# Kernel optimization log

Hardware: AMD Instinct MI355X
Metric: run time of the kernel (lower is better)

Reference implementation:

```python
import jax, jax.numpy as jnp
import numpy as np

B, NP, D, K, H = 2, 512, 768, 64, 8
HD = D // H  # head dim = 96


def layernorm(x, g, b, eps=1e-5):
    m = jnp.mean(x, axis=-1, keepdims=True)
    v = jnp.mean((x - m) ** 2, axis=-1, keepdims=True)
    return (x - m) / jnp.sqrt(v + eps) * g + b


def setup_inputs() -> dict:
    key = jax.random.key(0)
    ks = jax.random.split(key, 16)
    s = 0.02
    return {
        "features": jax.random.normal(ks[0], (B, NP, D), jnp.float32),
        "points_xyz": jax.random.normal(ks[1], (B, NP, 3), jnp.float32),
        # distance_encoder: Linear(1 -> D)
        "Wd": jax.random.normal(ks[2], (D,), jnp.float32) * s,
        "bd": jnp.zeros((D,), jnp.float32),
        # geo_attention: MultiheadAttention(D, H)
        "Wq": jax.random.normal(ks[3], (D, D), jnp.float32) * s,
        "bq": jnp.zeros((D,), jnp.float32),
        "Wk": jax.random.normal(ks[4], (D, D), jnp.float32) * s,
        "bk": jnp.zeros((D,), jnp.float32),
        "Wv": jax.random.normal(ks[5], (D, D), jnp.float32) * s,
        "bv": jnp.zeros((D,), jnp.float32),
        "Wo": jax.random.normal(ks[6], (D, D), jnp.float32) * s,
        "bo": jnp.zeros((D,), jnp.float32),
        # spatial_enhancer: Linear(2D -> D) + LayerNorm + SiLU
        "We": jax.random.normal(ks[7], (2 * D, D), jnp.float32) * s,
        "be": jnp.zeros((D,), jnp.float32),
        "g_ln": jnp.ones((D,), jnp.float32),
        "b_ln": jnp.zeros((D,), jnp.float32),
    }


def reference(features, points_xyz, Wd, bd, Wq, bq, Wk, bk, Wv, bv, Wo, bo, We, be, g_ln, b_ln):
    # pairwise distances per batch: [B, Np, Np]
    sq = jnp.sum(points_xyz ** 2, axis=-1)
    d2 = sq[:, :, None] + sq[:, None, :] - 2.0 * jnp.einsum("bnd,bmd->bnm", points_xyz, points_xyz)
    dist = jnp.sqrt(jnp.maximum(d2, 0.0))
    # k nearest neighbors (smallest distances)
    neg_d, idx = jax.lax.top_k(-dist, K)          # idx: [B, Np, K]
    nbr_dist = -neg_d                              # [B, Np, K]
    # gather neighbor features: [B, Np, K, D]
    nbr_feat = jax.vmap(lambda f, i: f[i])(features, idx)
    # distance encoder: Linear(1->D) on unsqueezed distances
    dist_feat = nbr_dist[..., None] * Wd + bd      # [B, Np, K, D]
    kv = nbr_feat + dist_feat
    # multi-head attention: per-point query over its K neighbors
    q = (features @ Wq + bq).reshape(B, NP, H, HD)
    k = (kv @ Wk + bk).reshape(B, NP, K, H, HD)
    v = (kv @ Wv + bv).reshape(B, NP, K, H, HD)
    scores = jnp.einsum("bnhd,bnkhd->bnhk", q, k) / jnp.sqrt(jnp.float32(HD))
    attn = jax.nn.softmax(scores, axis=-1)
    o = jnp.einsum("bnhk,bnkhd->bnhd", attn, v).reshape(B, NP, D)
    attended = o @ Wo + bo                          # [B, Np, D]
    # spatial enhancer on [features ; attended]
    ctx = jnp.concatenate([features, attended], axis=-1)
    enhanced = jax.nn.silu(layernorm(ctx @ We + be, g_ln, b_ln))
    return enhanced
```

## Files before the change

### kernel.cpp

```cpp
#include <hip/hip_runtime.h>
#include <math.h>

#define NPTS 512
#define DIM  768
#define KNN  64
#define NH   8
#define HDIM 96
#define MROWS 1024
#define MPAD  1088
#define WOROWS 832
#define WSQ   ((size_t)DIM * DIM)

typedef unsigned short u16;
typedef __attribute__((ext_vector_type(8))) short short8;
typedef __attribute__((ext_vector_type(4))) float f32x4;

__device__ __forceinline__ unsigned f2bf(float f) {
    unsigned u = __float_as_uint(f);
    return (u + 0x7fffu + ((u >> 16) & 1u)) >> 16;
}
__device__ __forceinline__ float bf2f(u16 v) {
    return __uint_as_float(((unsigned)v) << 16);
}

__global__ __launch_bounds__(256) void mega_prep_k(
    const float* __restrict__ features,
    const float* __restrict__ Wd, const float* __restrict__ bd,
    const float* __restrict__ Wq, const float* __restrict__ Wk, const float* __restrict__ Wv,
    const float* __restrict__ Wo, const float* __restrict__ bo, const float* __restrict__ We,
    u16* __restrict__ Fb, u16* __restrict__ Wob, u16* __restrict__ W3)
{
    __shared__ float T[64][65];
    int bid = blockIdx.x, tid = threadIdx.x;

    if (bid < 768) {
        int i = (bid * 256 + tid) * 4;
        float4 v = *(const float4*)&features[i];
        uint2 o;
        o.x = f2bf(v.x) | (f2bf(v.y) << 16);
        o.y = f2bf(v.z) | (f2bf(v.w) << 16);
        *(uint2*)&Fb[i] = o;
        return;
    }
    if (bid < 816) {
        int flat = (bid - 768) * 1024 + tid * 4;
        int r = flat / DIM, c = flat - r * DIM;
        uint2 o; o.x = 0u; o.y = 0u;
        if (r == 0) {
            float4 v = *(const float4*)&Wd[c];
            o.x = f2bf(v.x) | (f2bf(v.y) << 16);
            o.y = f2bf(v.z) | (f2bf(v.w) << 16);
        } else if (r == 1) {
            float4 v = *(const float4*)&bd[c];
            o.x = f2bf(v.x) | (f2bf(v.y) << 16);
            o.y = f2bf(v.z) | (f2bf(v.w) << 16);
        }
        *(uint2*)&Fb[(size_t)(MROWS + r) * DIM + c] = o;
        return;
    }
    if (bid < 1440) {
        int flat = (bid - 816) * 1024 + tid * 4;
        int r = flat / DIM, c = flat - r * DIM;
        uint2 o; o.x = 0u; o.y = 0u;
        if (r < DIM) {
            float4 v = *(const float4*)&Wo[(size_t)r * DIM + c];
            o.x = f2bf(v.x) | (f2bf(v.y) << 16);
            o.y = f2bf(v.z) | (f2bf(v.w) << 16);
        } else if (r == DIM) {
            float4 v = *(const float4*)&bo[c];
            o.x = f2bf(v.x) | (f2bf(v.y) << 16);
            o.y = f2bf(v.z) | (f2bf(v.w) << 16);
        }
        *(uint2*)&Wob[(size_t)r * DIM + c] = o;
        return;
    }
    {
        int t = bid - 1440;
        int m = t / 144, r2 = t % 144;
        int by = r2 / 12, bx = r2 % 12;
        const float* S = (m == 0) ? Wq : (m == 1) ? Wk : (m == 2) ? Wv
                       : (m == 3) ? We : (We + WSQ);
        u16* D = W3 + (size_t)m * WSQ;
        int r0 = by * 64, c0 = bx * 64;
#pragma unroll
        for (int i = 0; i < 16; ++i) {
            int lin = tid + i * 256;
            int r = lin >> 6, c = lin & 63;
            T[r][c] = S[(size_t)(r0 + r) * DIM + c0 + c];
        }
        __syncthreads();
#pragma unroll
        for (int i = 0; i < 16; ++i) {
            int lin = tid + i * 256;
            int c = lin >> 6, r = lin & 63;
            D[(size_t)(c0 + c) * DIM + r0 + r] = (u16)f2bf(T[r][c]);
        }
    }
}

union alignas(16) GTSm {
    struct { short As[64][72]; short Bs[64][72]; } g;
    struct { float P[NPTS * 3]; unsigned long long keys[NPTS]; } tk;
};

__global__ __launch_bounds__(256) void qkvw_topk_k(
    const u16* __restrict__ Fb, const u16* __restrict__ Wob, const u16* __restrict__ W3,
    const float* __restrict__ bq, const float* __restrict__ pts,
    float* __restrict__ FQ, u16* __restrict__ FKb, u16* __restrict__ FVb,
    u16* __restrict__ WeffT, float* __restrict__ c_e,
    int* __restrict__ idxb, float* __restrict__ distb)
{
    __shared__ GTSm sm;
    int bid = blockIdx.x, tid = threadIdx.x;

    if (bid >= 816) {
        int bn = bid - 816;
        int b  = bn >> 9;
        int n  = bn & (NPTS - 1);
        const float* pb = pts + (size_t)b * NPTS * 3;
        for (int i = tid; i < NPTS * 3; i += 256) sm.tk.P[i] = pb[i];
        __syncthreads();
        float xn = sm.tk.P[n * 3], yn = sm.tk.P[n * 3 + 1], zn = sm.tk.P[n * 3 + 2];
        float sqn = xn * xn + yn * yn + zn * zn;
        for (int m = tid; m < NPTS; m += 256) {
            float xm = sm.tk.P[m * 3], ym = sm.tk.P[m * 3 + 1], zm = sm.tk.P[m * 3 + 2];
            float sqm = xm * xm + ym * ym + zm * zm;
            float d2 = sqn + sqm - 2.0f * (xn * xm + yn * ym + zn * zm);
            float dist = sqrtf(fmaxf(d2, 0.0f));
            sm.tk.keys[m] = (((unsigned long long)__float_as_uint(dist)) << 32) | (unsigned)m;
        }
        __syncthreads();
        for (int k = 2; k <= NPTS; k <<= 1) {
            for (int j = k >> 1; j > 0; j >>= 1) {
                for (int i = tid; i < NPTS; i += 256) {
                    int ixj = i ^ j;
                    if (ixj > i) {
                        bool asc = ((i & k) == 0);
                        unsigned long long a = sm.tk.keys[i], bb = sm.tk.keys[ixj];
                        if ((a > bb) == asc) { sm.tk.keys[i] = bb; sm.tk.keys[ixj] = a; }
                    }
                }
                __syncthreads();
            }
        }
        if (tid < KNN) {
            unsigned long long kk = sm.tk.keys[tid];
            idxb[(size_t)bn * KNN + tid]  = (int)(kk & 0xffffffffu);
            distb[(size_t)bn * KNN + tid] = __uint_as_float((unsigned)(kk >> 32));
        }
        return;
    }

    int z   = bid / 204;
    int rem = bid - z * 204;
    int by  = rem / 12;
    int bx  = rem - by * 12;
    if (z == 0 && by >= 16) return;
    if (z == 3 && by >= 13) return;
    const u16* A  = (z == 3) ? Wob : Fb;
    const u16* BT = W3 + (size_t)((z == 3) ? 4 : z) * WSQ;

    int wave = tid >> 6, lane = tid & 63;
    int wr = (wave >> 1) * 32, wc = (wave & 1) * 32;
    int l15 = lane & 15, kg = lane >> 4;
    int brow = by * 64, bcol = bx * 64;

    f32x4 acc[2][2] = {};

    int srow = tid >> 3;
    int scol = (tid & 7) * 8;

    for (int k0 = 0; k0 < DIM; k0 += 64) {
#pragma unroll
        for (int s = 0; s < 2; ++s) {
            int r = srow + s * 32;
            *(short8*)&sm.g.As[r][scol] = *(const short8*)&A[(size_t)(brow + r) * DIM + k0 + scol];
            *(short8*)&sm.g.Bs[r][scol] = *(const short8*)&BT[(size_t)(bcol + r) * DIM + k0 + scol];
        }
        __syncthreads();
#pragma unroll
        for (int kk = 0; kk < 2; ++kk) {
            short8 a0 = *(const short8*)&sm.g.As[wr + l15][kk * 32 + kg * 8];
            short8 a1 = *(const short8*)&sm.g.As[wr + 16 + l15][kk * 32 + kg * 8];
            short8 b0 = *(const short8*)&sm.g.Bs[wc + l15][kk * 32 + kg * 8];
            short8 b1 = *(const short8*)&sm.g.Bs[wc + 16 + l15][kk * 32 + kg * 8];
            acc[0][0] = __builtin_amdgcn_mfma_f32_16x16x32_bf16(a0, b0, acc[0][0], 0, 0, 0);
            acc[0][1] = __builtin_amdgcn_mfma_f32_16x16x32_bf16(a0, b1, acc[0][1], 0, 0, 0);
            acc[1][0] = __builtin_amdgcn_mfma_f32_16x16x32_bf16(a1, b0, acc[1][0], 0, 0, 0);
            acc[1][1] = __builtin_amdgcn_mfma_f32_16x16x32_bf16(a1, b1, acc[1][1], 0, 0, 0);
        }
        __syncthreads();
    }

#pragma unroll
    for (int m = 0; m < 2; ++m) {
#pragma unroll
        for (int n = 0; n < 2; ++n) {
            int col  = bcol + wc + n * 16 + l15;
            int row0 = brow + wr + m * 16 + kg * 4;
            if (z == 0) {
                float bv = bq[col];
#pragma unroll
                for (int j = 0; j < 4; ++j)
                    FQ[(size_t)(row0 + j) * DIM + col] = acc[m][n][j] + bv;
            } else if (z == 1) {
#pragma unroll
                for (int j = 0; j < 4; ++j)
                    FKb[(size_t)(row0 + j) * DIM + col] = (u16)f2bf(acc[m][n][j]);
            } else if (z == 2) {
#pragma unroll
                for (int j = 0; j < 4; ++j)
                    FVb[(size_t)(row0 + j) * DIM + col] = (u16)f2bf(acc[m][n][j]);
            } else {
                if (row0 + 3 < DIM) {
                    unsigned long long pk =
                          (unsigned long long)f2bf(acc[m][n][0])
                        | ((unsigned long long)f2bf(acc[m][n][1]) << 16)
                        | ((unsigned long long)f2bf(acc[m][n][2]) << 32)
                        | ((unsigned long long)f2bf(acc[m][n][3]) << 48);
                    *(unsigned long long*)&WeffT[(size_t)col * DIM + row0] = pk;
                } else {
#pragma unroll
                    for (int j = 0; j < 4; ++j) {
                        int row = row0 + j;
                        if (row < DIM)       WeffT[(size_t)col * DIM + row] = (u16)f2bf(acc[m][n][j]);
                        else if (row == DIM) c_e[col] = acc[m][n][j];
                    }
                }
            }
        }
    }
}

__global__ __launch_bounds__(256) void gemm_final_k(
    const u16* __restrict__ Fb, const u16* __restrict__ Ob,
    const u16* __restrict__ WeTopT, const u16* __restrict__ WeffT,
    const float* __restrict__ c_e, const float* __restrict__ be,
    float* __restrict__ Z0, float* __restrict__ Z1)
{
    int z = blockIdx.z;
    const u16*   A    = z ? Ob : Fb;
    const u16*   BT   = z ? WeffT : WeTopT;
    const float* bias = z ? c_e : be;
    float*       Z    = z ? Z1 : Z0;

    __shared__ short As[64][72];
    __shared__ short Bs[64][72];

    int tid  = threadIdx.x;
    int wave = tid >> 6, lane = tid & 63;
    int wr = (wave >> 1) * 32, wc = (wave & 1) * 32;
    int l15 = lane & 15, kg = lane >> 4;
    int brow = blockIdx.y * 64, bcol = blockIdx.x * 64;

    f32x4 acc[2][2] = {};

    int srow = tid >> 3;
    int scol = (tid & 7) * 8;

    for (int k0 = 0; k0 < DIM; k0 += 64) {
#pragma unroll
        for (int s = 0; s < 2; ++s) {
            int r = srow + s * 32;
            *(short8*)&As[r][scol] = *(const short8*)&A[(size_t)(brow + r) * DIM + k0 + scol];
            *(short8*)&Bs[r][scol] = *(const short8*)&BT[(size_t)(bcol + r) * DIM + k0 + scol];
        }
        __syncthreads();
#pragma unroll
        for (int kk = 0; kk < 2; ++kk) {
            short8 a0 = *(const short8*)&As[wr + l15][kk * 32 + kg * 8];
            short8 a1 = *(const short8*)&As[wr + 16 + l15][kk * 32 + kg * 8];
            short8 b0 = *(const short8*)&Bs[wc + l15][kk * 32 + kg * 8];
            short8 b1 = *(const short8*)&Bs[wc + 16 + l15][kk * 32 + kg * 8];
            acc[0][0] = __builtin_amdgcn_mfma_f32_16x16x32_bf16(a0, b0, acc[0][0], 0, 0, 0);
            acc[0][1] = __builtin_amdgcn_mfma_f32_16x16x32_bf16(a0, b1, acc[0][1], 0, 0, 0);
            acc[1][0] = __builtin_amdgcn_mfma_f32_16x16x32_bf16(a1, b0, acc[1][0], 0, 0, 0);
            acc[1][1] = __builtin_amdgcn_mfma_f32_16x16x32_bf16(a1, b1, acc[1][1], 0, 0, 0);
        }
        __syncthreads();
    }

#pragma unroll
    for (int m = 0; m < 2; ++m) {
#pragma unroll
        for (int n = 0; n < 2; ++n) {
            int col = bcol + wc + n * 16 + l15;
            float bv = bias[col];
#pragma unroll
            for (int j = 0; j < 4; ++j) {
                int row = brow + wr + m * 16 + kg * 4 + j;
                Z[(size_t)row * DIM + col] = acc[m][n][j] + bv;
            }
        }
    }
}

__global__ __launch_bounds__(512) void attn_k(
    const float* __restrict__ FQ, const u16* __restrict__ FKb, const u16* __restrict__ FVb,
    const int* __restrict__ idxb, const float* __restrict__ distb,
    const float* __restrict__ bk, const float* __restrict__ bv,
    u16* __restrict__ O)
{
    int bn = blockIdx.x;
    int b  = bn >> 9;
    int tid = threadIdx.x;
    int wv = tid >> 6, lane = tid & 63;

    __shared__ float qlds[NH][104];
    __shared__ int   s_idx[KNN];
    __shared__ float s_dist[KNN];
    __shared__ float s_sc[NH][68];
    __shared__ float s_att[NH][68];
    __shared__ float s_qh[NH][2];
    __shared__ float s_sd[NH];

    if (tid < KNN) {
        s_idx[tid]  = idxb[(size_t)bn * KNN + tid];
        s_dist[tid] = distb[(size_t)bn * KNN + tid];
    }
    const float* qrow = FQ + (size_t)bn * DIM;
    {
        int d = tid;
        if (d < DIM) qlds[d / HDIM][d % HDIM] = qrow[d];
        int d2 = tid + 512;
        if (d2 < DIM) qlds[d2 / HDIM][d2 % HDIM] = qrow[d2];
    }
    __syncthreads();

    {
        int h = wv;
        const u16* wdk = FKb + (size_t)MROWS * DIM + h * HDIM;
        const u16* ckr = FKb + (size_t)(MROWS + 1) * DIM + h * HDIM;
        const float* bkh = bk + h * HDIM;
        float q = qlds[h][lane];
        float pw = q * bf2f(wdk[lane]);
        float pc = q * (bf2f(ckr[lane]) + bkh[lane]);
        if (lane < HDIM - 64) {
            float q2 = qlds[h][lane + 64];
            pw = fmaf(q2, bf2f(wdk[lane + 64]), pw);
            pc = fmaf(q2, bf2f(ckr[lane + 64]) + bkh[lane + 64], pc);
        }
#pragma unroll
        for (int off = 32; off; off >>= 1) {
            pw += __shfl_xor(pw, off);
            pc += __shfl_xor(pc, off);
        }
        if (lane == 0) { s_qh[h][0] = pw; s_qh[h][1] = pc; }
    }

    {
        int j = tid >> 3, h = tid & 7;
        const u16* kr = FKb + (size_t)(b * NPTS + s_idx[j]) * DIM + h * HDIM;
        const uint4* kr4 = (const uint4*)kr;
        float a0 = 0.f, a1 = 0.f, a2 = 0.f, a3 = 0.f;
#pragma unroll
        for (int i = 0; i < 12; ++i) {
            uint4 kv = kr4[i];
            float4 qa = *(const float4*)&qlds[h][i * 8];
            float4 qb = *(const float4*)&qlds[h][i * 8 + 4];
            a0 = fmaf(qa.x, __uint_as_float(kv.x << 16), a0);
            a1 = fmaf(qa.y, __uint_as_float(kv.x & 0xffff0000u), a1);
            a2 = fmaf(qa.z, __uint_as_float(kv.y << 16), a2);
            a3 = fmaf(qa.w, __uint_as_float(kv.y & 0xffff0000u), a3);
            a0 = fmaf(qb.x, __uint_as_float(kv.z << 16), a0);
            a1 = fmaf(qb.y, __uint_as_float(kv.z & 0xffff0000u), a1);
            a2 = fmaf(qb.z, __uint_as_float(kv.w << 16), a2);
            a3 = fmaf(qb.w, __uint_as_float(kv.w & 0xffff0000u), a3);
        }
        s_sc[h][j] = (a0 + a1) + (a2 + a3);
    }
    __syncthreads();

    {
        int h = wv, j = lane;
        const float invs = 0.10206207261596575f;
        float qwdk = s_qh[h][0], qck = s_qh[h][1];
        float dj = s_dist[j];
        float sc = (s_sc[h][j] + dj * qwdk + qck) * invs;
        float mx = sc;
#pragma unroll
        for (int off = 32; off; off >>= 1) mx = fmaxf(mx, __shfl_xor(mx, off));
        float ev = __expf(sc - mx);
        float sum = ev;
#pragma unroll
        for (int off = 32; off; off >>= 1) sum += __shfl_xor(sum, off);
        float att = ev / sum;
        s_att[h][j] = att;
        float sd = att * dj;
#pragma unroll
        for (int off = 32; off; off >>= 1) sd += __shfl_xor(sd, off);
        if (lane == 0) s_sd[h] = sd;
    }
    __syncthreads();

    if (tid < 384) {
        int d0 = tid * 2;
        int h  = d0 / HDIM;
        const float* attp = s_att[h];
        const size_t basev = (size_t)(b * NPTS) * DIM + d0;
        float o0 = 0.f, o1 = 0.f;
#pragma unroll 4
        for (int j = 0; j < KNN; ++j) {
            unsigned pv = *(const unsigned*)&FVb[basev + (size_t)s_idx[j] * DIM];
            float a = attp[j];
            o0 = fmaf(a, __uint_as_float(pv << 16), o0);
            o1 = fmaf(a, __uint_as_float(pv & 0xffff0000u), o1);
        }
        const u16* wdv = FVb + (size_t)MROWS * DIM;
        const u16* cvr = FVb + (size_t)(MROWS + 1) * DIM;
        float sdh = s_sd[h];
        o0 += sdh * bf2f(wdv[d0])     + (bf2f(cvr[d0])     + bv[d0]);
        o1 += sdh * bf2f(wdv[d0 + 1]) + (bf2f(cvr[d0 + 1]) + bv[d0 + 1]);
        unsigned po = f2bf(o0) | (f2bf(o1) << 16);
        *(unsigned*)&O[(size_t)bn * DIM + d0] = po;
    }
}

__global__ __launch_bounds__(256) void ln_silu_k(
    const float* __restrict__ Z0, const float* __restrict__ Z1,
    const float* __restrict__ g, const float* __restrict__ bta,
    float* __restrict__ out)
{
    int bn = blockIdx.x, tid = threadIdx.x;
    const float* z0 = Z0 + (size_t)bn * DIM;
    const float* z1 = Z1 + (size_t)bn * DIM;
    int e0 = tid * 3;
    float x0 = z0[e0] + z1[e0];
    float x1 = z0[e0 + 1] + z1[e0 + 1];
    float x2 = z0[e0 + 2] + z1[e0 + 2];
    float s = x0 + x1 + x2;
    float ss = x0 * x0 + x1 * x1 + x2 * x2;
    __shared__ float red[4][2];
#pragma unroll
    for (int off = 32; off; off >>= 1) {
        s  += __shfl_xor(s, off);
        ss += __shfl_xor(ss, off);
    }
    int w = tid >> 6;
    if ((tid & 63) == 0) { red[w][0] = s; red[w][1] = ss; }
    __syncthreads();
    s  = red[0][0] + red[1][0] + red[2][0] + red[3][0];
    ss = red[0][1] + red[1][1] + red[2][1] + red[3][1];
    float mean = s * (1.0f / DIM);
    float var  = ss * (1.0f / DIM) - mean * mean;
    float rstd = rsqrtf(var + 1e-5f);
    float* orow = out + (size_t)bn * DIM;
#pragma unroll
    for (int i = 0; i < 3; ++i) {
        int e = e0 + i;
        float x = (i == 0) ? x0 : (i == 1) ? x1 : x2;
        float y = (x - mean) * rstd * g[e] + bta[e];
        orow[e] = y / (1.0f + __expf(-y));
    }
}

extern "C" void kernel_launch(void* const* d_in, const int* in_sizes, int n_in,
                              void* d_out, int out_size, void* d_ws, size_t ws_size,
                              hipStream_t stream)
{
    const float* features = (const float*)d_in[0];
    const float* pts      = (const float*)d_in[1];
    const float* Wd       = (const float*)d_in[2];
    const float* bd       = (const float*)d_in[3];
    const float* Wq       = (const float*)d_in[4];
    const float* bq       = (const float*)d_in[5];
    const float* Wk       = (const float*)d_in[6];
    const float* bk       = (const float*)d_in[7];
    const float* Wv       = (const float*)d_in[8];
    const float* bv       = (const float*)d_in[9];
    const float* Wo       = (const float*)d_in[10];
    const float* bo       = (const float*)d_in[11];
    const float* We       = (const float*)d_in[12];
    const float* be       = (const float*)d_in[13];
    const float* g_ln     = (const float*)d_in[14];
    const float* b_ln     = (const float*)d_in[15];

    const size_t MAT  = (size_t)MROWS * DIM;
    const size_t MATP = (size_t)MPAD  * DIM;

    float* ws = (float*)d_ws;
    float* FQ    = ws;
    u16*   FKb   = (u16*)(ws + MATP);
    u16*   FVb   = FKb + MATP;
    u16*   Fb    = FVb + MATP;
    u16*   Ob    = Fb + MATP;
    u16*   Wob   = Ob + MAT;
    u16*   W3    = Wob + (size_t)WOROWS * DIM;
    u16*   WeffT = W3 + 5 * WSQ;
    float* c_e   = (float*)(WeffT + WSQ);
    int*   idxb  = (int*)(c_e + DIM);
    float* distb = (float*)(idxb + (size_t)MROWS * KNN);
    float* Z0    = FQ;
    float* Z1    = (float*)FKb;

    mega_prep_k<<<2160, 256, 0, stream>>>(features, Wd, bd, Wq, Wk, Wv, Wo, bo, We,
                                          Fb, Wob, W3);
    qkvw_topk_k<<<1840, 256, 0, stream>>>(
        Fb, Wob, W3, bq, pts, FQ, FKb, FVb, WeffT, c_e, idxb, distb);
    attn_k<<<MROWS, 512, 0, stream>>>(FQ, FKb, FVb, idxb, distb, bk, bv, Ob);
    gemm_final_k<<<dim3(12, 16, 2), 256, 0, stream>>>(
        Fb, Ob, W3 + 3 * WSQ, WeffT, c_e, be, Z0, Z1);
    ln_silu_k<<<MROWS, 256, 0, stream>>>(Z0, Z1, g_ln, b_ln, (float*)d_out);
}
```

Baseline: 78.98 us.

## Move features@We_top GEMM into qkv kernel and split-K the attended GEMM

The Z0 = features·We_top + be GEMM does not depend on attention, so it moves into the earlier qkv/topk kernel as a fifth z-slice, overlapping with the other independent work. The remaining O·Weff GEMM is split four ways along K into separate partial buffers, which gives more blocks on the device. LayerNorm then sums the four partials, Z0 and c_e with float4 loads using 192 threads. This costs extra workspace and extra global traffic for the partial sums.

```diff
diff --git a/kernel.cpp b/kernel.cpp
--- a/kernel.cpp
+++ b/kernel.cpp
@@ -105,16 +105,17 @@
 
 __global__ __launch_bounds__(256) void qkvw_topk_k(
     const u16* __restrict__ Fb, const u16* __restrict__ Wob, const u16* __restrict__ W3,
-    const float* __restrict__ bq, const float* __restrict__ pts,
+    const float* __restrict__ bq, const float* __restrict__ be,
+    const float* __restrict__ pts,
     float* __restrict__ FQ, u16* __restrict__ FKb, u16* __restrict__ FVb,
-    u16* __restrict__ WeffT, float* __restrict__ c_e,
+    u16* __restrict__ WeffT, float* __restrict__ c_e, float* __restrict__ Z0,
     int* __restrict__ idxb, float* __restrict__ distb)
 {
     __shared__ GTSm sm;
     int bid = blockIdx.x, tid = threadIdx.x;
 
-    if (bid >= 816) {
-        int bn = bid - 816;
+    if (bid >= 1008) {
+        int bn = bid - 1008;
         int b  = bn >> 9;
         int n  = bn & (NPTS - 1);
         const float* pb = pts + (size_t)b * NPTS * 3;
@@ -151,14 +152,20 @@
         return;
     }
 
-    int z   = bid / 204;
-    int rem = bid - z * 204;
-    int by  = rem / 12;
-    int bx  = rem - by * 12;
-    if (z == 0 && by >= 16) return;
-    if (z == 3 && by >= 13) return;
+    int z, by, bx;
+    if (bid < 816) {
+        z = bid / 204;
+        int rem = bid - z * 204;
+        by = rem / 12; bx = rem - by * 12;
+        if (z == 0 && by >= 16) return;
+        if (z == 3 && by >= 13) return;
+    } else {
+        z = 4;
+        int rem = bid - 816;
+        by = rem / 12; bx = rem - by * 12;
+    }
     const u16* A  = (z == 3) ? Wob : Fb;
-    const u16* BT = W3 + (size_t)((z == 3) ? 4 : z) * WSQ;
+    const u16* BT = W3 + (size_t)((z == 3) ? 4 : (z == 4) ? 3 : z) * WSQ;
 
     int wave = tid >> 6, lane = tid & 63;
     int wr = (wave >> 1) * 32, wc = (wave & 1) * 32;
@@ -211,6 +218,11 @@
 #pragma unroll
                 for (int j = 0; j < 4; ++j)
                     FVb[(size_t)(row0 + j) * DIM + col] = (u16)f2bf(acc[m][n][j]);
+            } else if (z == 4) {
+                float bv = be[col];
+#pragma unroll
+                for (int j = 0; j < 4; ++j)
+                    Z0[(size_t)(row0 + j) * DIM + col] = acc[m][n][j] + bv;
             } else {
                 if (row0 + 3 < DIM) {
                     unsigned long long pk =
@@ -232,18 +244,10 @@
     }
 }
 
-__global__ __launch_bounds__(256) void gemm_final_k(
-    const u16* __restrict__ Fb, const u16* __restrict__ Ob,
-    const u16* __restrict__ WeTopT, const u16* __restrict__ WeffT,
-    const float* __restrict__ c_e, const float* __restrict__ be,
-    float* __restrict__ Z0, float* __restrict__ Z1)
+__global__ __launch_bounds__(256) void gemm_z1_k(
+    const u16* __restrict__ Ob, const u16* __restrict__ WeffT,
+    float* __restrict__ P)
 {
-    int z = blockIdx.z;
-    const u16*   A    = z ? Ob : Fb;
-    const u16*   BT   = z ? WeffT : WeTopT;
-    const float* bias = z ? c_e : be;
-    float*       Z    = z ? Z1 : Z0;
-
     __shared__ short As[64][72];
     __shared__ short Bs[64][72];
 
@@ -252,18 +256,19 @@
     int wr = (wave >> 1) * 32, wc = (wave & 1) * 32;
     int l15 = lane & 15, kg = lane >> 4;
     int brow = blockIdx.y * 64, bcol = blockIdx.x * 64;
+    int kbeg = blockIdx.z * 192;
 
     f32x4 acc[2][2] = {};
 
     int srow = tid >> 3;
     int scol = (tid & 7) * 8;
 
-    for (int k0 = 0; k0 < DIM; k0 += 64) {
+    for (int k0 = kbeg; k0 < kbeg + 192; k0 += 64) {
 #pragma unroll
         for (int s = 0; s < 2; ++s) {
             int r = srow + s * 32;
-            *(short8*)&As[r][scol] = *(const short8*)&A[(size_t)(brow + r) * DIM + k0 + scol];
-            *(short8*)&Bs[r][scol] = *(const short8*)&BT[(size_t)(bcol + r) * DIM + k0 + scol];
+            *(short8*)&As[r][scol] = *(const short8*)&Ob[(size_t)(brow + r) * DIM + k0 + scol];
+            *(short8*)&Bs[r][scol] = *(const short8*)&WeffT[(size_t)(bcol + r) * DIM + k0 + scol];
         }
         __syncthreads();
 #pragma unroll
@@ -280,16 +285,16 @@
         __syncthreads();
     }
 
+    float* Pz = P + (size_t)blockIdx.z * MROWS * DIM;
 #pragma unroll
     for (int m = 0; m < 2; ++m) {
 #pragma unroll
         for (int n = 0; n < 2; ++n) {
             int col = bcol + wc + n * 16 + l15;
-            float bv = bias[col];
 #pragma unroll
             for (int j = 0; j < 4; ++j) {
                 int row = brow + wr + m * 16 + kg * 4 + j;
-                Z[(size_t)row * DIM + col] = acc[m][n][j] + bv;
+                Pz[(size_t)row * DIM + col] = acc[m][n][j];
             }
         }
     }
@@ -416,21 +421,28 @@
     }
 }
 
-__global__ __launch_bounds__(256) void ln_silu_k(
-    const float* __restrict__ Z0, const float* __restrict__ Z1,
+__global__ __launch_bounds__(192) void ln_silu_k(
+    const float* __restrict__ Z0, const float* __restrict__ P,
+    const float* __restrict__ c_e,
     const float* __restrict__ g, const float* __restrict__ bta,
     float* __restrict__ out)
 {
     int bn = blockIdx.x, tid = threadIdx.x;
-    const float* z0 = Z0 + (size_t)bn * DIM;
-    const float* z1 = Z1 + (size_t)bn * DIM;
-    int e0 = tid * 3;
-    float x0 = z0[e0] + z1[e0];
-    float x1 = z0[e0 + 1] + z1[e0 + 1];
-    float x2 = z0[e0 + 2] + z1[e0 + 2];
-    float s = x0 + x1 + x2;
-    float ss = x0 * x0 + x1 * x1 + x2 * x2;
-    __shared__ float red[4][2];
+    size_t ro = (size_t)bn * DIM;
+    int e0 = tid * 4;
+    float4 x = *(const float4*)&Z0[ro + e0];
+#pragma unroll
+    for (int z = 0; z < 4; ++z) {
+        float4 p = *(const float4*)&P[(size_t)z * MROWS * DIM + ro + e0];
+        x.x += p.x; x.y += p.y; x.z += p.z; x.w += p.w;
+    }
+    {
+        float4 c = *(const float4*)&c_e[e0];
+        x.x += c.x; x.y += c.y; x.z += c.z; x.w += c.w;
+    }
+    float s  = (x.x + x.y) + (x.z + x.w);
+    float ss = (x.x * x.x + x.y * x.y) + (x.z * x.z + x.w * x.w);
+    __shared__ float red[3][2];
 #pragma unroll
     for (int off = 32; off; off >>= 1) {
         s  += __shfl_xor(s, off);
@@ -439,19 +451,24 @@
     int w = tid >> 6;
     if ((tid & 63) == 0) { red[w][0] = s; red[w][1] = ss; }
     __syncthreads();
-    s  = red[0][0] + red[1][0] + red[2][0] + red[3][0];
-    ss = red[0][1] + red[1][1] + red[2][1] + red[3][1];
+    s  = red[0][0] + red[1][0] + red[2][0];
+    ss = red[0][1] + red[1][1] + red[2][1];
     float mean = s * (1.0f / DIM);
     float var  = ss * (1.0f / DIM) - mean * mean;
     float rstd = rsqrtf(var + 1e-5f);
-    float* orow = out + (size_t)bn * DIM;
-#pragma unroll
-    for (int i = 0; i < 3; ++i) {
-        int e = e0 + i;
-        float x = (i == 0) ? x0 : (i == 1) ? x1 : x2;
-        float y = (x - mean) * rstd * g[e] + bta[e];
-        orow[e] = y / (1.0f + __expf(-y));
-    }
+    float4 gv = *(const float4*)&g[e0];
+    float4 bv = *(const float4*)&bta[e0];
+    float4 y;
+    y.x = (x.x - mean) * rstd * gv.x + bv.x;
+    y.y = (x.y - mean) * rstd * gv.y + bv.y;
+    y.z = (x.z - mean) * rstd * gv.z + bv.z;
+    y.w = (x.w - mean) * rstd * gv.w + bv.w;
+    float4 o;
+    o.x = y.x / (1.0f + __expf(-y.x));
+    o.y = y.y / (1.0f + __expf(-y.y));
+    o.z = y.z / (1.0f + __expf(-y.z));
+    o.w = y.w / (1.0f + __expf(-y.w));
+    *(float4*)&out[ro + e0] = o;
 }
 
 extern "C" void kernel_launch(void* const* d_in, const int* in_sizes, int n_in,
@@ -490,15 +507,14 @@
     float* c_e   = (float*)(WeffT + WSQ);
     int*   idxb  = (int*)(c_e + DIM);
     float* distb = (float*)(idxb + (size_t)MROWS * KNN);
-    float* Z0    = FQ;
-    float* Z1    = (float*)FKb;
+    float* Z0    = distb + (size_t)MROWS * KNN;
+    float* Pbuf  = Z0 + MAT;
 
     mega_prep_k<<<2160, 256, 0, stream>>>(features, Wd, bd, Wq, Wk, Wv, Wo, bo, We,
                                           Fb, Wob, W3);
-    qkvw_topk_k<<<1840, 256, 0, stream>>>(
-        Fb, Wob, W3, bq, pts, FQ, FKb, FVb, WeffT, c_e, idxb, distb);
+    qkvw_topk_k<<<2032, 256, 0, stream>>>(
+        Fb, Wob, W3, bq, be, pts, FQ, FKb, FVb, WeffT, c_e, Z0, idxb, distb);
     attn_k<<<MROWS, 512, 0, stream>>>(FQ, FKb, FVb, idxb, distb, bk, bv, Ob);
-    gemm_final_k<<<dim3(12, 16, 2), 256, 0, stream>>>(
-        Fb, Ob, W3 + 3 * WSQ, WeffT, c_e, be, Z0, Z1);
-    ln_silu_k<<<MROWS, 256, 0, stream>>>(Z0, Z1, g_ln, b_ln, (float*)d_out);
-}
+    gemm_z1_k<<<dim3(12, 16, 4), 256, 0, stream>>>(Ob, WeffT, Pbuf);
+    ln_silu_k<<<MROWS, 192, 0, stream>>>(Z0, Pbuf, c_e, g_ln, b_ln, (float*)d_out);
+}
```

New measurement: 85.07 us. +7.7%, slower.
